# Kernel optimization log

Measured on AMD Instinct MI355X. Metric: run time of the kernel, lower is better.

## Reference

```python
import jax, jax.numpy as jnp
import numpy as np

B_SCENES = 2; K = 5; C = 128; H = 64; W = 64
D_INNER = C; D_STATE = 16; DT_RANK = 8
C_TUKEY = 0.3; ALPHA = 2.0; BETA = 0.4; GAMMA = 0.8


def affine_grid(theta, Ho, Wo):
    # torch F.affine_grid, align_corners=False (pixel centers)
    xs = (jnp.arange(Wo, dtype=jnp.float32) + 0.5) * (2.0 / Wo) - 1.0
    ys = (jnp.arange(Ho, dtype=jnp.float32) + 0.5) * (2.0 / Ho) - 1.0
    gx, gy = jnp.meshgrid(xs, ys)
    base = jnp.stack([gx, gy, jnp.ones_like(gx)], axis=-1)  # (H,W,3)
    return jnp.einsum('nij,hwj->nhwi', theta, base)  # (N,H,W,2)


def grid_sample(src, grid):
    # bilinear, zero padding, align_corners=False; src (N,C,H,W), grid (N,H,W,2)
    N, Cc, Hs, Ws = src.shape
    ix = ((grid[..., 0] + 1.0) * Ws - 1.0) * 0.5
    iy = ((grid[..., 1] + 1.0) * Hs - 1.0) * 0.5
    x0 = jnp.floor(ix); y0 = jnp.floor(iy)
    def tap(xf, yf):
        v = ((xf >= 0) & (xf <= Ws - 1) & (yf >= 0) & (yf <= Hs - 1)).astype(src.dtype)
        xc = jnp.clip(xf, 0, Ws - 1).astype(jnp.int32)
        yc = jnp.clip(yf, 0, Hs - 1).astype(jnp.int32)
        vals = jax.vmap(lambda s, y, x: s[:, y, x])(src, yc, xc)  # (N,C,H,W)
        return vals * v[:, None]
    wx1 = (ix - x0)[:, None]; wy1 = (iy - y0)[:, None]
    wx0 = 1.0 - wx1; wy0 = 1.0 - wy1
    return (tap(x0, y0) * wx0 * wy0 + tap(x0 + 1.0, y0) * wx1 * wy0
            + tap(x0, y0 + 1.0) * wx0 * wy1 + tap(x0 + 1.0, y0 + 1.0) * wx1 * wy1)


def ss2d(tokens, in_proj_w, conv_w, conv_b, x_proj_w, dt_w, dt_b, A_logs, Ds, ln_g, ln_b, out_proj_w):
    # tokens (C, Hs, Ws) channel-first; VMamba-style v05_noz core, d_inner=C
    xin = jnp.einsum('chw,dc->dhw', tokens, in_proj_w)
    xc = jax.lax.conv_general_dilated(xin[None], conv_w, (1, 1), [(1, 1), (1, 1)],
                                      dimension_numbers=('NCHW', 'OIHW', 'NCHW'),
                                      feature_group_count=D_INNER)[0] + conv_b[:, None, None]
    xa = jax.nn.silu(xc)
    d, Hs, Ws = xa.shape
    L = Hs * Ws
    x_hw = xa.reshape(d, L)
    x_wh = jnp.swapaxes(xa, 1, 2).reshape(d, L)
    xs = jnp.stack([x_hw, x_wh, x_hw[:, ::-1], x_wh[:, ::-1]], axis=0)  # (4,d,L)
    x_dbl = jnp.einsum('kdl,kcd->kcl', xs, x_proj_w)
    dt = x_dbl[:, :DT_RANK]
    Bm = x_dbl[:, DT_RANK:DT_RANK + D_STATE]
    Cm = x_dbl[:, DT_RANK + D_STATE:]
    dts = jax.nn.softplus(jnp.einsum('kdr,krl->kdl', dt_w, dt) + dt_b[..., None])
    A = -jnp.exp(A_logs)  # (4,d,n)
    seq = (jnp.moveaxis(xs, -1, 0), jnp.moveaxis(dts, -1, 0),
           jnp.moveaxis(Bm, -1, 0), jnp.moveaxis(Cm, -1, 0))
    def step(h, inp):
        xt, dtt, Bt, Ct = inp
        h = h * jnp.exp(dtt[..., None] * A) + (dtt * xt)[..., None] * Bt[:, None, :]
        return h, jnp.einsum('kdn,kn->kd', h, Ct)
    h0 = jnp.zeros((4, d, D_STATE), tokens.dtype)
    _, ys = jax.lax.scan(jax.checkpoint(step), h0, seq)  # ys (L,4,d)
    ys = jnp.moveaxis(ys, 0, -1) + Ds[..., None] * xs  # (4,d,L)
    untr = lambda y: jnp.swapaxes(y.reshape(d, Ws, Hs), 1, 2).reshape(d, L)
    y = ys[0] + untr(ys[1]) + ys[2][:, ::-1] + untr(ys[3][:, ::-1])
    yt = y.T  # (L,d)
    mu = yt.mean(-1, keepdims=True)
    var = ((yt - mu) ** 2).mean(-1, keepdims=True)
    yn = (yt - mu) * jax.lax.rsqrt(var + 1e-5) * ln_g + ln_b
    out = yn @ out_proj_w.T  # (L,C)
    return jnp.moveaxis(out.reshape(Hs, Ws, -1), -1, 0)  # (C,Hs,Ws)


def forward(x, nam, in_proj_w, conv_w, conv_b, x_proj_w, dt_w, dt_b, A_logs, Ds, ln_g, ln_b, out_proj_w):
    xg = x.reshape(B_SCENES, K, C, H, W)  # record_len is constant K
    t_rows = nam[:, 0]  # ego row i=0 of t_matrix: (B,K,2,3)
    def scene(xb, t_row):
        warped = grid_sample(xb, affine_grid(t_row, H, W))  # (K,C,H,W)
        ego = warped[0]
        # per-pixel cosine sim across channels (F.normalize(dim=0) on (C,HW) views)
        en = ego / jnp.maximum(jnp.sqrt((ego ** 2).sum(0, keepdims=True)), 1e-6)
        nb = warped / jnp.maximum(jnp.sqrt((warped ** 2).sum(1, keepdims=True)), 1e-6)
        sims = jnp.clip((en[None] * nb).sum(1), -1.0, 1.0)  # (K,H,W)
        r = jnp.maximum(1.0 - sims, 0.0)
        xr = jnp.maximum(r / C_TUKEY, 0.0)
        w_pix = jnp.maximum(jnp.maximum(1.0 - xr * xr, 0.0) ** 2, 1e-6)[:, None]  # (K,1,H,W)
        tx = t_row[:, 0, 2]; ty = t_row[:, 1, 2]
        yaw = jnp.abs(jnp.arctan2(t_row[:, 0, 1], t_row[:, 0, 0]))
        g = jax.nn.sigmoid(ALPHA - BETA * jnp.sqrt(tx ** 2 + ty ** 2) - GAMMA * yaw)  # (K,)
        logit = jnp.log(w_pix + 1e-8) + jnp.log(g + 1e-8)[:, None, None, None]
        alpha = jax.nn.softmax(logit, axis=0)  # softmax over K per pixel
        weighted = warped * alpha
        tokens = jnp.swapaxes(weighted.reshape(K, C, H * W), 0, 1)  # (C,K,HW)
        out = ss2d(tokens, in_proj_w, conv_w, conv_b, x_proj_w, dt_w, dt_b,
                   A_logs, Ds, ln_g, ln_b, out_proj_w)  # (C,K,HW)
        return jnp.swapaxes(out, 0, 1).reshape(K, C, W, H)[0]  # (C,W,H) as in original view
    return jax.vmap(scene)(xg, t_rows)


def setup_inputs() -> dict:
    key = jax.random.key(0)
    ks = jax.random.split(key, 10)
    x = jax.random.normal(ks[0], (B_SCENES * K, C, H, W), jnp.float32)
    record_len = jnp.full((B_SCENES,), K, dtype=jnp.int32)
    eye = jnp.broadcast_to(jnp.array([[1.0, 0.0, 0.0], [0.0, 1.0, 0.0]], jnp.float32),
                           (B_SCENES, K, K, 2, 3))
    nam = eye + 0.05 * jax.random.normal(ks[1], (B_SCENES, K, K, 2, 3), jnp.float32)
    in_proj_w = 0.05 * jax.random.normal(ks[2], (D_INNER, C), jnp.float32)
    conv_w = 0.1 * jax.random.normal(ks[3], (D_INNER, 1, 3, 3), jnp.float32)
    conv_b = jnp.zeros((D_INNER,), jnp.float32)
    x_proj_w = 0.05 * jax.random.normal(ks[4], (4, DT_RANK + 2 * D_STATE, D_INNER), jnp.float32)
    dt_w = 0.1 * jax.random.normal(ks[5], (4, D_INNER, DT_RANK), jnp.float32)
    dt_b = -4.6 + 0.5 * jax.random.normal(ks[6], (4, D_INNER), jnp.float32)
    A_logs = jnp.broadcast_to(jnp.log(jnp.arange(1, D_STATE + 1, dtype=jnp.float32)),
                              (4, D_INNER, D_STATE)) + jnp.zeros((4, D_INNER, D_STATE), jnp.float32)
    Ds = jnp.ones((4, D_INNER), jnp.float32)
    ln_g = jnp.ones((D_INNER,), jnp.float32)
    ln_b = jnp.zeros((D_INNER,), jnp.float32)
    out_proj_w = 0.05 * jax.random.normal(ks[7], (C, D_INNER), jnp.float32)
    return {"x": x, "record_len": record_len, "normalized_affine_matrix": nam,
            "in_proj_w": in_proj_w, "conv_w": conv_w, "conv_b": conv_b,
            "x_proj_w": x_proj_w, "dt_w": dt_w, "dt_b": dt_b, "A_logs": A_logs,
            "Ds": Ds, "ln_g": ln_g, "ln_b": ln_b, "out_proj_w": out_proj_w}


def reference(x, record_len, normalized_affine_matrix, in_proj_w, conv_w, conv_b,
              x_proj_w, dt_w, dt_b, A_logs, Ds, ln_g, ln_b, out_proj_w):
    # record_len is a constant (= K per scene) and only determines the static grouping
    return forward(x, normalized_affine_matrix, in_proj_w, conv_w, conv_b,
                   x_proj_w, dt_w, dt_b, A_logs, Ds, ln_g, ln_b, out_proj_w)
```

## Files before the change

kernel.cpp:

```cpp
#include <hip/hip_runtime.h>
#include <math.h>

#define B_S   2
#define PIX   4096
#define LL    20480
#define NS    16
#define RR    8
#define NCHK  512
#define LC    40
#define SUBS  10
#define NSUB  4
#define NGRP  32
#define GCH   16
#define K0CP  52

typedef float v2f __attribute__((ext_vector_type(2)));

__device__ __forceinline__ v2f pk_mul(v2f a, v2f b) {
  v2f d;
  asm("v_pk_mul_f32 %0, %1, %2" : "=v"(d) : "v"(a), "v"(b));
  return d;
}
#define PK_FMA_ACC(a, b, c) asm("v_pk_fma_f32 %0, %1, %2, %0" : "+v"(a) : "v"(b), "v"(c))
#define PK_DECAY(h, e, m) asm("v_pk_fma_f32 %0, %0, %1, %2" : "+v"(h) : "v"(e), "v"(m))

template<int K>
__device__ __forceinline__ int zmapT(int l) {
  if (K == 0) return l;
  if (K == 1) return ((l % 5) << 12) + l / 5;
  if (K == 2) return 20479 - l;
  int lr = 20479 - l;
  return ((lr % 5) << 12) + lr / 5;
}

__global__ __launch_bounds__(256)
void k_warp(const float* __restrict__ x, const float* __restrict__ nam,
            float* __restrict__ warped) {
  int g = blockIdx.x * 256 + threadIdx.x;
  int p  = g & 4095;
  int c  = (g >> 12) & 127;
  int bk = g >> 19;
  int b = bk / 5, k = bk - b * 5;
  const float* th = nam + (size_t)(b * 25 + k) * 6;
  float gx = ((p & 63) + 0.5f) * 0.03125f - 1.0f;
  float gy = ((p >> 6) + 0.5f) * 0.03125f - 1.0f;
  float grx = th[0] * gx + th[1] * gy + th[2];
  float gry = th[3] * gx + th[4] * gy + th[5];
  float ix = ((grx + 1.0f) * 64.0f - 1.0f) * 0.5f;
  float iy = ((gry + 1.0f) * 64.0f - 1.0f) * 0.5f;
  float x0 = floorf(ix), y0 = floorf(iy);
  float fx = ix - x0,  fy = iy - y0;
  const float* src = x + (size_t)(bk * 128 + c) * PIX;
  float acc = 0.0f;
  #pragma unroll
  for (int dy = 0; dy < 2; ++dy) {
    float yf = y0 + dy;
    float wy = dy ? fy : 1.0f - fy;
    if (yf < 0.0f || yf > 63.0f) continue;
    int yi = (int)yf;
    #pragma unroll
    for (int dx = 0; dx < 2; ++dx) {
      float xf = x0 + dx;
      float wx = dx ? fx : 1.0f - fx;
      if (xf < 0.0f || xf > 63.0f) continue;
      acc += wx * wy * src[yi * 64 + (int)xf];
    }
  }
  warped[g] = acc;
}

__global__ __launch_bounds__(512)
void k_alpha(const float* __restrict__ warped, const float* __restrict__ nam,
             float* __restrict__ alpha) {
  __shared__ float part[8][64][9];
  int blk = blockIdx.x;
  int b = blk >> 6;
  int p0 = (blk & 63) << 6;
  int wv = threadIdx.x >> 6, lane = threadIdx.x & 63;
  int p = p0 + lane;
  const float* wb = warped + (size_t)b * 5 * 128 * PIX + p;
  float dot[5] = {0,0,0,0,0}, ssq[5] = {0,0,0,0,0};
  int c0 = wv * 16;
  for (int c = c0; c < c0 + 16; ++c) {
    float w0 = wb[(size_t)c * PIX];
    ssq[0] += w0 * w0;
    #pragma unroll
    for (int k = 1; k < 5; ++k) {
      float wk = wb[((size_t)k * 128 + c) * PIX];
      dot[k] += w0 * wk;
      ssq[k] += wk * wk;
    }
  }
  part[wv][lane][0] = ssq[0];
  #pragma unroll
  for (int k = 1; k < 5; ++k) {
    part[wv][lane][k] = dot[k];
    part[wv][lane][4 + k] = ssq[k];
  }
  __syncthreads();
  if (threadIdx.x < 64) {
    float q[9];
    #pragma unroll
    for (int j = 0; j < 9; ++j) {
      float s = 0.0f;
      #pragma unroll
      for (int w = 0; w < 8; ++w) s += part[w][lane][j];
      q[j] = s;
    }
    float n0 = fmaxf(sqrtf(q[0]), 1e-6f);
    float logit[5];
    #pragma unroll
    for (int k = 0; k < 5; ++k) {
      float dotk = (k == 0) ? q[0] : q[k];
      float ssqk = (k == 0) ? q[0] : q[4 + k];
      float nk = fmaxf(sqrtf(ssqk), 1e-6f);
      float sim = fminf(fmaxf(dotk / (n0 * nk), -1.0f), 1.0f);
      float r = fmaxf(1.0f - sim, 0.0f);
      float xr = r * (1.0f / 0.3f);
      float tt = fmaxf(1.0f - xr * xr, 0.0f);
      float wp = fmaxf(tt * tt, 1e-6f);
      const float* th = nam + (size_t)(b * 25 + k) * 6;
      float tx = th[2], ty = th[5];
      float yaw = fabsf(atan2f(th[1], th[0]));
      float gk = 1.0f / (1.0f + __expf(-(2.0f - 0.4f * sqrtf(tx*tx + ty*ty) - 0.8f * yaw)));
      logit[k] = __logf(wp + 1e-8f) + __logf(gk + 1e-8f);
    }
    float m = logit[0];
    #pragma unroll
    for (int k = 1; k < 5; ++k) m = fmaxf(m, logit[k]);
    float e[5], s = 0.0f;
    #pragma unroll
    for (int k = 0; k < 5; ++k) { e[k] = __expf(logit[k] - m); s += e[k]; }
    float inv = 1.0f / s;
    #pragma unroll
    for (int k = 0; k < 5; ++k)
      alpha[((size_t)(b * 5 + k)) * PIX + p] = e[k] * inv;
  }
}

__global__ __launch_bounds__(256, 4)
void k_gemm_in(const float* __restrict__ warped, const float* __restrict__ alpha,
               const float* __restrict__ W, float* __restrict__ X0) {
  __shared__ float xl[64][129];
  __shared__ __align__(16) float wlT[32][132];
  int t = threadIdx.x;
  int row0 = blockIdx.x * 64;
  int b = row0 / LL;
  int z0 = row0 - b * LL;
  int a = z0 >> 12;
  int p0 = z0 & 4095;
  int ba = b * 5 + a;
  int r = t & 63, cg = t >> 6;
  float av = alpha[(size_t)ba * PIX + p0 + r];
  #pragma unroll
  for (int i = 0; i < 32; ++i) {
    int c = cg * 32 + i;
    xl[r][c] = warped[((size_t)ba * 128 + c) * PIX + p0 + r] * av;
  }
  int zl2 = t & 31;
  int mg  = t >> 5;
  float acc0[16], acc1[16];
  #pragma unroll
  for (int i = 0; i < 16; ++i) { acc0[i] = 0.0f; acc1[i] = 0.0f; }
  for (int c0 = 0; c0 < 128; c0 += 32) {
    __syncthreads();
    #pragma unroll
    for (int i = 0; i < 16; ++i) {
      int m = (t >> 5) * 16 + i;
      wlT[t & 31][m] = W[(size_t)m * 128 + c0 + (t & 31)];
    }
    __syncthreads();
    const float* xr0 = xl[2 * zl2];
    const float* xr1 = xl[2 * zl2 + 1];
    for (int cc = 0; cc < 32; ++cc) {
      float xv0 = xr0[c0 + cc];
      float xv1 = xr1[c0 + cc];
      const float4* wr = (const float4*)(&wlT[cc][mg * 16]);
      #pragma unroll
      for (int q = 0; q < 4; ++q) {
        float4 w4 = wr[q];
        acc0[q*4+0] = fmaf(w4.x, xv0, acc0[q*4+0]);
        acc0[q*4+1] = fmaf(w4.y, xv0, acc0[q*4+1]);
        acc0[q*4+2] = fmaf(w4.z, xv0, acc0[q*4+2]);
        acc0[q*4+3] = fmaf(w4.w, xv0, acc0[q*4+3]);
        acc1[q*4+0] = fmaf(w4.x, xv1, acc1[q*4+0]);
        acc1[q*4+1] = fmaf(w4.y, xv1, acc1[q*4+1]);
        acc1[q*4+2] = fmaf(w4.z, xv1, acc1[q*4+2]);
        acc1[q*4+3] = fmaf(w4.w, xv1, acc1[q*4+3]);
      }
    }
  }
  __syncthreads();
  #pragma unroll
  for (int q = 0; q < 16; ++q) {
    xl[2 * zl2][mg * 16 + q] = acc0[q];
    xl[2 * zl2 + 1][mg * 16 + q] = acc1[q];
  }
  __syncthreads();
  #pragma unroll
  for (int i = 0; i < 32; ++i) {
    int idx = i * 256 + t;
    X0[((size_t)row0 + (idx >> 7)) * 128 + (idx & 127)] = xl[idx >> 7][idx & 127];
  }
}

__global__ __launch_bounds__(256)
void k_conv(const float* __restrict__ X0, const float* __restrict__ cw,
            const float* __restrict__ cb, float* __restrict__ XT) {
  int g = blockIdx.x * 256 + threadIdx.x;
  int d = g & 127;
  int zz4 = g >> 7;
  int b = zz4 / (LL / 4);
  int r = zz4 - b * (LL / 4);
  int z0 = r * 4;
  int a = z0 >> 12, p = z0 & 4095;
  float w9[9];
  #pragma unroll
  for (int i = 0; i < 9; ++i) w9[i] = cw[d * 9 + i];
  float cbv = cb[d];
  float acc[4] = {cbv, cbv, cbv, cbv};
  #pragma unroll
  for (int di = 0; di < 3; ++di) {
    int aa = a + di - 1;
    if (aa < 0 || aa >= 5) continue;
    const float* rowb = X0 + ((size_t)b * LL + (size_t)aa * PIX) * 128 + d;
    #pragma unroll
    for (int dj = -1; dj <= 4; ++dj) {
      int pp = p + dj;
      if (pp < 0 || pp >= PIX) continue;
      float v = rowb[(size_t)pp * 128];
      #pragma unroll
      for (int o = 0; o < 4; ++o) {
        int rel = dj - o;
        if (rel >= -1 && rel <= 1) acc[o] = fmaf(w9[di * 3 + rel + 1], v, acc[o]);
      }
    }
  }
  float* dst = XT + (size_t)(zz4 * 4) * 128 + d;
  #pragma unroll
  for (int o = 0; o < 4; ++o) {
    float sg = 1.0f / (1.0f + __expf(-acc[o]));
    dst[(size_t)o * 128] = acc[o] * sg;
  }
}

__global__ __launch_bounds__(256, 4)
void k_gemmZ(const float* __restrict__ X, const float* __restrict__ W,
             float* __restrict__ ZdtB, float* __restrict__ ZC) {
  __shared__ float xl[64][129];
  __shared__ __align__(16) float wlT[32][164];
  int t = threadIdx.x;
  int row0 = blockIdx.x * 64;
  #pragma unroll
  for (int i = 0; i < 32; ++i) {
    int idx = i * 256 + t;
    xl[idx >> 7][idx & 127] = X[((size_t)row0 + (idx >> 7)) * 128 + (idx & 127)];
  }
  int zl2 = t & 31;
  int mg  = t >> 5;
  float acc0[20], acc1[20];
  #pragma unroll
  for (int i = 0; i < 20; ++i) { acc0[i] = 0.0f; acc1[i] = 0.0f; }
  for (int c0 = 0; c0 < 128; c0 += 32) {
    __syncthreads();
    #pragma unroll
    for (int i = 0; i < 20; ++i) {
      int m = (t >> 5) * 20 + i;
      wlT[t & 31][m] = W[(size_t)m * 128 + c0 + (t & 31)];
    }
    __syncthreads();
    const float* xr0 = xl[2 * zl2];
    const float* xr1 = xl[2 * zl2 + 1];
    for (int cc = 0; cc < 32; ++cc) {
      float xv0 = xr0[c0 + cc];
      float xv1 = xr1[c0 + cc];
      const float4* wr = (const float4*)(&wlT[cc][mg * 20]);
      #pragma unroll
      for (int q = 0; q < 5; ++q) {
        float4 w4 = wr[q];
        acc0[q*4+0] = fmaf(w4.x, xv0, acc0[q*4+0]);
        acc0[q*4+1] = fmaf(w4.y, xv0, acc0[q*4+1]);
        acc0[q*4+2] = fmaf(w4.z, xv0, acc0[q*4+2]);
        acc0[q*4+3] = fmaf(w4.w, xv0, acc0[q*4+3]);
        acc1[q*4+0] = fmaf(w4.x, xv1, acc1[q*4+0]);
        acc1[q*4+1] = fmaf(w4.y, xv1, acc1[q*4+1]);
        acc1[q*4+2] = fmaf(w4.z, xv1, acc1[q*4+2]);
        acc1[q*4+3] = fmaf(w4.w, xv1, acc1[q*4+3]);
      }
    }
  }
  int dir = mg >> 1;
  int halfc = mg & 1;
  #pragma unroll
  for (int rr = 0; rr < 2; ++rr) {
    const float* acc = rr ? acc1 : acc0;
    int row = row0 + 2 * zl2 + rr;
    int b = row / LL, z = row - b * LL;
    int a = z >> 12, qq = z & 4095;
    int l;
    if (dir == 0)      l = z;
    else if (dir == 1) l = 5 * qq + a;
    else if (dir == 2) l = 20479 - z;
    else               l = 20479 - (5 * qq + a);
    size_t seqrow = (size_t)(b * 4 + dir) * LL + l;
    if (halfc == 0) {
      float* dD = ZdtB + seqrow * 24;
      #pragma unroll
      for (int q2 = 0; q2 < 5; ++q2)
        *(float4*)(dD + q2 * 4) = make_float4(acc[q2*4], acc[q2*4+1], acc[q2*4+2], acc[q2*4+3]);
    } else {
      float* dD = ZdtB + seqrow * 24;
      *(float4*)(dD + 20) = make_float4(acc[0], acc[1], acc[2], acc[3]);
      float* dC = ZC + seqrow * 16;
      #pragma unroll
      for (int q2 = 0; q2 < 4; ++q2)
        *(float4*)(dC + q2 * 4) = make_float4(acc[4+q2*4], acc[4+q2*4+1], acc[4+q2*4+2], acc[4+q2*4+3]);
    }
  }
}

template<int K>
__device__ void scan_body(int b, int chunk, int dh, int lane,
    const float* __restrict__ XT, const float* __restrict__ ZdtB,
    const float* __restrict__ ZC,
    const float* __restrict__ dt_w, const float* __restrict__ dt_b,
    const float* __restrict__ A_logs, const float* __restrict__ Ds,
    float* __restrict__ h_out, float* __restrict__ sumdts,
    float* __restrict__ ysz, float* __restrict__ cumdtv,
    float* stD, float* stC, float* xs)
{
  const int d = dh * 64 + lane;
  const int kd = K * 128 + d;
  bool chainok = true;
  #pragma unroll
  for (int n = 0; n < NS; ++n) {
    float An = -__expf(A_logs[(size_t)kd * 16 + n]);
    chainok = chainok && (fabsf(An + (float)(n + 1)) < 3e-5f * (float)(n + 1));
  }
  v2f dw2[4];
  #pragma unroll
  for (int r = 0; r < 4; ++r) {
    dw2[r][0] = dt_w[(size_t)kd * 8 + 2 * r];
    dw2[r][1] = dt_w[(size_t)kd * 8 + 2 * r + 1];
  }
  const float dtb = dt_b[kd], dsv = Ds[kd];
  v2f h2[8];
  #pragma unroll
  for (int n = 0; n < 8; ++n) h2[n] = (v2f){0.0f, 0.0f};
  float sdt = 0.0f;
  const int seq = b * 4 + K;
  const float* ZDs = ZdtB + (size_t)seq * LL * 24;
  const float* ZCs = ZC + (size_t)seq * LL * 16;
  const float* Xb = XT + (size_t)b * LL * 128;
  float* ysb = ysz + (size_t)seq * PIX * 128;
  float* cdb = cumdtv + (size_t)seq * PIX * 128;
  const int l0 = chunk * LC;

  if (__all(chainok ? 1 : 0)) {
    #pragma unroll 1
    for (int sub = 0; sub < NSUB; ++sub) {
      const int ls = l0 + sub * SUBS;
      {
        const v2f* srcD = (const v2f*)(ZDs + (size_t)ls * 24);
        v2f* dstD = (v2f*)stD;
        #pragma unroll
        for (int i = 0; i < 2; ++i) {
          int idx = i * 64 + lane;
          if (idx < SUBS * 12) dstD[idx] = srcD[idx];
        }
      }
      int s0c = 0;
      bool needC;
      if (K == 0)      needC = (ls < PIX);
      else if (K == 2) needC = (ls + SUBS > LL - PIX);
      else             needC = true;
      if (K == 1) s0c = (5 - (ls % 5)) % 5;
      if (K == 3) s0c = (9 - (ls % 5)) % 5;
      if (needC) {
        if (K == 0 || K == 2) {
          const v2f* srcC = (const v2f*)(ZCs + (size_t)ls * 16);
          v2f* dstC = (v2f*)stC;
          #pragma unroll
          for (int i = 0; i < 2; ++i) {
            int idx = i * 64 + lane;
            if (idx < SUBS * 8) dstC[idx] = srcC[idx];
          }
        } else {
          int j = lane >> 4, col = lane & 15;
          if (j < 2) {
            int l = ls + s0c + 5 * j;
            if (l > LL - 1) l = LL - 1;
            stC[lane] = ZCs[(size_t)l * 16 + col];
          }
        }
      }
      #pragma unroll
      for (int s = 0; s < SUBS; ++s) {
        int z = zmapT<K>(ls + s);
        xs[s * 64 + lane] = Xb[(size_t)z * 128 + d];
      }
      int zc = 0;
      if (K == 1) zc = (ls + s0c) / 5;
      if (K == 3) zc = (20479 - ls - s0c) / 5;
      int yj = 0;
      #pragma unroll
      for (int s = 0; s < SUBS; ++s) {
        const v2f* rowD = (const v2f*)(stD + s * 24);
        v2f zd0 = rowD[0], zd1 = rowD[1], zd2 = rowD[2], zd3 = rowD[3];
        v2f da = pk_mul(dw2[0], zd0);
        PK_FMA_ACC(da, dw2[1], zd1);
        PK_FMA_ACC(da, dw2[2], zd2);
        PK_FMA_ACC(da, dw2[3], zd3);
        float dtl = dtb + da[0] + da[1];
        float edt = __expf(dtl);
        float e1 = __builtin_amdgcn_rcpf(1.0f + edt);
        float dt = (dtl > 20.0f) ? dtl : __logf(1.0f + edt);
        sdt += dt;
        float xsv = xs[s * 64 + lane];
        float dtx = dt * xsv;
        v2f dtx2 = {dtx, dtx};
        float e2 = e1 * e1;
        v2f E[8];
        E[0] = (v2f){e1, e2};
        v2f e2s = {e2, e2};
        E[1] = pk_mul(E[0], e2s);
        E[2] = pk_mul(E[1], e2s);
        E[3] = pk_mul(E[2], e2s);
        float e8 = E[3][1];
        v2f e8s = {e8, e8};
        E[4] = pk_mul(E[0], e8s);
        E[5] = pk_mul(E[1], e8s);
        E[6] = pk_mul(E[2], e8s);
        E[7] = pk_mul(E[3], e8s);
        const v2f* B2 = (const v2f*)(stD + s * 24 + 8);
        #pragma unroll
        for (int i = 0; i < 8; ++i) {
          v2f m = pk_mul(dtx2, B2[i]);
          PK_DECAY(h2[i], E[i], m);
        }
        bool doY;
        int z;
        if (K == 0)      { z = ls + s;            doY = (z < PIX); }
        else if (K == 2) { z = 20479 - (ls + s);  doY = (z < PIX); }
        else             { z = zc;                doY = ((s % 5) == s0c); }
        if (doY) {
          const v2f* C2 = (const v2f*)(stC + ((K == 0 || K == 2) ? s : yj) * 16);
          v2f ya = pk_mul(h2[0], C2[0]);
          #pragma unroll
          for (int i = 1; i < 8; ++i) PK_FMA_ACC(ya, h2[i], C2[i]);
          float y = fmaf(dsv, xsv, ya[0] + ya[1]);
          size_t o = (size_t)z * 128 + d;
          ysb[o] = y;
          cdb[o] = sdt;
          ++yj;
          if (K == 1) ++zc;
          if (K == 3) --zc;
        }
      }
    }
  } else {
    float An[NS];
    #pragma unroll
    for (int n = 0; n < NS; ++n) An[n] = -__expf(A_logs[(size_t)kd * 16 + n]);
    float hs[NS];
    #pragma unroll
    for (int n = 0; n < NS; ++n) hs[n] = 0.0f;
    #pragma unroll 1
    for (int l = l0; l < l0 + LC; ++l) {
      int z = zmapT<K>(l);
      const float* rowD = ZDs + (size_t)l * 24;
      float dtl = dtb;
      #pragma unroll
      for (int r = 0; r < RR; ++r) dtl += dt_w[(size_t)kd * 8 + r] * rowD[r];
      float edt = __expf(dtl);
      float dt = (dtl > 20.0f) ? dtl : __logf(1.0f + edt);
      sdt += dt;
      float xv = Xb[(size_t)z * 128 + d];
      float dtx = dt * xv;
      #pragma unroll
      for (int n = 0; n < NS; ++n)
        hs[n] = hs[n] * __expf(dt * An[n]) + dtx * rowD[8 + n];
      if (z < PIX) {
        const float* rowC = ZCs + (size_t)l * 16;
        float y = dsv * xv;
        #pragma unroll
        for (int n = 0; n < NS; ++n) y = fmaf(hs[n], rowC[n], y);
        size_t o = (size_t)z * 128 + d;
        ysb[o] = y;
        cdb[o] = sdt;
      }
    }
    #pragma unroll
    for (int n = 0; n < 8; ++n) h2[n] = (v2f){hs[2*n], hs[2*n+1]};
  }
  float* ho = h_out + (((size_t)seq * NCHK + chunk) * 128 + d) * 16;
  #pragma unroll
  for (int n = 0; n < 8; ++n) {
    ho[2*n] = h2[n][0];
    ho[2*n+1] = h2[n][1];
  }
  sumdts[((size_t)seq * NCHK + chunk) * 128 + d] = sdt;
}

__global__ __launch_bounds__(256, 6)
void k_scan1(const float* __restrict__ XT, const float* __restrict__ ZdtB,
             const float* __restrict__ ZC,
             const float* __restrict__ dt_w, const float* __restrict__ dt_b,
             const float* __restrict__ A_logs, const float* __restrict__ Ds,
             float* __restrict__ h_out, float* __restrict__ sumdts,
             float* __restrict__ ysz, float* __restrict__ cumdtv) {
  __shared__ __align__(16) float stD_all[4][SUBS * 24];
  __shared__ __align__(16) float stC_all[4][SUBS * 16];
  __shared__ __align__(16) float xs_all[4][SUBS * 64];
  int tid = threadIdx.x, wid = tid >> 6, lane = tid & 63;
  int bid = blockIdx.x;
  int bb = bid / (K0CP + 768);
  int idx = bid - bb * (K0CP + 768);
  int k, cp;
  if (idx < K0CP)            { k = 0; cp = idx; }
  else if (idx < K0CP + 256) { k = 1; cp = idx - K0CP; }
  else if (idx < K0CP + 512) { k = 2; cp = idx - (K0CP + 256); }
  else                       { k = 3; cp = idx - (K0CP + 512); }
  int chunk = cp * 2 + (wid >> 1);
  int dh = wid & 1;
  float* stD = stD_all[wid];
  float* stC = stC_all[wid];
  float* xs  = xs_all[wid];
  switch (k) {
    case 0: scan_body<0>(bb, chunk, dh, lane, XT, ZdtB, ZC, dt_w, dt_b, A_logs, Ds, h_out, sumdts, ysz, cumdtv, stD, stC, xs); break;
    case 1: scan_body<1>(bb, chunk, dh, lane, XT, ZdtB, ZC, dt_w, dt_b, A_logs, Ds, h_out, sumdts, ysz, cumdtv, stD, stC, xs); break;
    case 2: scan_body<2>(bb, chunk, dh, lane, XT, ZdtB, ZC, dt_w, dt_b, A_logs, Ds, h_out, sumdts, ysz, cumdtv, stD, stC, xs); break;
    default: scan_body<3>(bb, chunk, dh, lane, XT, ZdtB, ZC, dt_w, dt_b, A_logs, Ds, h_out, sumdts, ysz, cumdtv, stD, stC, xs); break;
  }
}

__global__ __launch_bounds__(256)
void k_comb_a(const float* __restrict__ A_logs, const float* __restrict__ sumdts,
              const float* __restrict__ h_out, float* __restrict__ Ag,
              float* __restrict__ Bg) {
  int g = blockIdx.x * 256 + threadIdx.x;
  int n = g & 15;
  int d = (g >> 4) & 127;
  int grp = (g >> 11) & 31;
  int seq = g >> 16;
  int k = seq & 3;
  float An = -__expf(A_logs[(size_t)(k * 128 + d) * 16 + n]);
  float A = 1.0f, Bv = 0.0f;
  size_t cbase = (size_t)seq * NCHK + grp * GCH;
  #pragma unroll 4
  for (int j = 0; j < GCH; ++j) {
    float a = __expf(An * sumdts[(cbase + j) * 128 + d]);
    float b = h_out[((cbase + j) * 128 + d) * 16 + n];
    A *= a;
    Bv = Bv * a + b;
  }
  size_t o = (((size_t)seq * NGRP + grp) * 128 + d) * 16 + n;
  Ag[o] = A;
  Bg[o] = Bv;
}

__global__ __launch_bounds__(256)
void k_comb_b(const float* __restrict__ Ag, const float* __restrict__ Bg,
              float* __restrict__ Hg) {
  int g = blockIdx.x * 256 + threadIdx.x;
  int n = g & 15;
  int d = (g >> 4) & 127;
  int seq = g >> 11;
  float H = 0.0f;
  #pragma unroll
  for (int grp = 0; grp < NGRP; ++grp) {
    size_t o = (((size_t)seq * NGRP + grp) * 128 + d) * 16 + n;
    Hg[o] = H;
    H = Ag[o] * H + Bg[o];
  }
}

__global__ __launch_bounds__(256)
void k_comb_c(const float* __restrict__ A_logs, const float* __restrict__ sumdts,
              const float* __restrict__ h_out, const float* __restrict__ Hg,
              float* __restrict__ h_in) {
  int g = blockIdx.x * 256 + threadIdx.x;
  int n = g & 15;
  int d = (g >> 4) & 127;
  int grp = (g >> 11) & 31;
  int seq = g >> 16;
  int k = seq & 3;
  float An = -__expf(A_logs[(size_t)(k * 128 + d) * 16 + n]);
  float h = Hg[(((size_t)seq * NGRP + grp) * 128 + d) * 16 + n];
  size_t cbase = (size_t)seq * NCHK + grp * GCH;
  #pragma unroll 4
  for (int j = 0; j < GCH; ++j) {
    size_t o = ((cbase + j) * 128 + d) * 16 + n;
    h_in[o] = h;
    float a = __expf(An * sumdts[(cbase + j) * 128 + d]);
    h = a * h + h_out[o];
  }
}

__global__ __launch_bounds__(256)
void k_wt(const float* __restrict__ Wo, float* __restrict__ WT) {
  __shared__ float tl[32][33];
  int bx = blockIdx.x & 3, by = blockIdx.x >> 2;
  int t = threadIdx.x;
  int tx = t & 31, ty = t >> 5;
  #pragma unroll
  for (int i = 0; i < 4; ++i)
    tl[ty + i * 8][tx] = Wo[(size_t)(by * 32 + ty + i * 8) * 128 + bx * 32 + tx];
  __syncthreads();
  #pragma unroll
  for (int i = 0; i < 4; ++i)
    WT[(size_t)(bx * 32 + ty + i * 8) * 128 + by * 32 + tx] = tl[tx][ty + i * 8];
}

__global__ __launch_bounds__(256)
void k_merge(const float* __restrict__ ysz, const float* __restrict__ ZC,
             const float* __restrict__ A_logs, const float* __restrict__ h_in,
             const float* __restrict__ cumdt,
             const float* __restrict__ ln_g, const float* __restrict__ ln_b,
             const float* __restrict__ WT, float* __restrict__ out) {
  __shared__ __align__(16) float ynT[128][20];
  __shared__ float red[4][8][2];
  int blk = blockIdx.x;
  int b = blk >> 8;
  int p0 = (blk & 255) * 16;
  int tid = threadIdx.x;
  int t = tid & 127;
  int half = tid >> 7;
  int w = tid >> 6;
  float g = ln_g[t], bb = ln_b[t];
  bool cok[4];
  #pragma unroll
  for (int k = 0; k < 4; ++k) {
    bool c = true;
    #pragma unroll
    for (int n = 0; n < NS; ++n) {
      float An = -__expf(A_logs[(size_t)(k * 128 + t) * 16 + n]);
      c = c && (fabsf(An + (float)(n + 1)) < 3e-5f * (float)(n + 1));
    }
    cok[k] = c;
  }
  float yv[8];
  #pragma unroll
  for (int i = 0; i < 8; ++i) {
    int p = p0 + 2 * i + half;
    float y = 0.0f;
    #pragma unroll
    for (int k = 0; k < 4; ++k) {
      size_t zi = ((size_t)(b * 4 + k) * PIX + p) * 128 + t;
      float yk = ysz[zi];
      int l;
      if (k == 0)      l = p;
      else if (k == 1) l = 5 * p;
      else if (k == 2) l = 20479 - p;
      else             l = 20479 - 5 * p;
      int chunk = l / LC;
      float cd = cumdt[zi];
      const v2f* hi2 = (const v2f*)(h_in + (((size_t)(b * 4 + k) * NCHK + chunk) * 128 + t) * 16);
      const v2f* Cr2 = (const v2f*)(ZC + ((size_t)(b * 4 + k) * LL + l) * 16);
      float fix;
      if (cok[k]) {
        float q = __expf(-cd);
        float q2 = q * q;
        v2f Q[8];
        Q[0] = (v2f){q, q2};
        v2f q2s = {q2, q2};
        Q[1] = pk_mul(Q[0], q2s);
        Q[2] = pk_mul(Q[1], q2s);
        Q[3] = pk_mul(Q[2], q2s);
        float q8 = Q[3][1];
        v2f q8s = {q8, q8};
        Q[4] = pk_mul(Q[0], q8s);
        Q[5] = pk_mul(Q[1], q8s);
        Q[6] = pk_mul(Q[2], q8s);
        Q[7] = pk_mul(Q[3], q8s);
        v2f a = pk_mul(pk_mul(hi2[0], Cr2[0]), Q[0]);
        #pragma unroll
        for (int j = 1; j < 8; ++j) {
          v2f m = pk_mul(hi2[j], Cr2[j]);
          PK_FMA_ACC(a, m, Q[j]);
        }
        fix = a[0] + a[1];
      } else {
        fix = 0.0f;
        const float* hi = (const float*)hi2;
        const float* Cr = (const float*)Cr2;
        #pragma unroll
        for (int n = 0; n < NS; ++n) {
          float An = -__expf(A_logs[(size_t)(k * 128 + t) * 16 + n]);
          fix += Cr[n] * hi[n] * __expf(An * cd);
        }
      }
      y += yk + fix;
    }
    yv[i] = y;
    float s1 = y, s2 = y * y;
    #pragma unroll
    for (int off = 32; off; off >>= 1) {
      s1 += __shfl_xor(s1, off);
      s2 += __shfl_xor(s2, off);
    }
    if ((tid & 63) == 0) { red[w][i][0] = s1; red[w][i][1] = s2; }
  }
  __syncthreads();
  #pragma unroll
  for (int i = 0; i < 8; ++i) {
    int pl = 2 * i + half;
    float S1 = red[half * 2][i][0] + red[half * 2 + 1][i][0];
    float S2 = red[half * 2][i][1] + red[half * 2 + 1][i][1];
    float mu = S1 * (1.0f / 128.0f);
    float var = S2 * (1.0f / 128.0f) - mu * mu;
    float rs = rsqrtf(var + 1e-5f);
    ynT[t][pl] = (yv[i] - mu) * rs * g + bb;
  }
  __syncthreads();
  float acc[8];
  #pragma unroll
  for (int i = 0; i < 8; ++i) acc[i] = 0.0f;
  for (int dd = 0; dd < 128; ++dd) {
    float wv = WT[(size_t)dd * 128 + t];
    const float4* yr = (const float4*)(&ynT[dd][half * 8]);
    float4 ya = yr[0], yb4 = yr[1];
    acc[0] = fmaf(ya.x,  wv, acc[0]);
    acc[1] = fmaf(ya.y,  wv, acc[1]);
    acc[2] = fmaf(ya.z,  wv, acc[2]);
    acc[3] = fmaf(ya.w,  wv, acc[3]);
    acc[4] = fmaf(yb4.x, wv, acc[4]);
    acc[5] = fmaf(yb4.y, wv, acc[5]);
    acc[6] = fmaf(yb4.z, wv, acc[6]);
    acc[7] = fmaf(yb4.w, wv, acc[7]);
  }
  float* dst = out + ((size_t)b * 128 + t) * PIX + p0 + half * 8;
  *(float4*)(dst)     = make_float4(acc[0], acc[1], acc[2], acc[3]);
  *(float4*)(dst + 4) = make_float4(acc[4], acc[5], acc[6], acc[7]);
}

extern "C" void kernel_launch(void* const* d_in, const int* in_sizes, int n_in,
                              void* d_out, int out_size, void* d_ws, size_t ws_size,
                              hipStream_t stream) {
  const float* x         = (const float*)d_in[0];
  const float* nam       = (const float*)d_in[2];
  const float* in_proj_w = (const float*)d_in[3];
  const float* conv_w    = (const float*)d_in[4];
  const float* conv_b    = (const float*)d_in[5];
  const float* x_proj_w  = (const float*)d_in[6];
  const float* dt_w      = (const float*)d_in[7];
  const float* dt_b      = (const float*)d_in[8];
  const float* A_logs    = (const float*)d_in[9];
  const float* Ds        = (const float*)d_in[10];
  const float* ln_g      = (const float*)d_in[11];
  const float* ln_b      = (const float*)d_in[12];
  const float* out_proj_w= (const float*)d_in[13];
  float* out = (float*)d_out;
  float* ws  = (float*)d_ws;

  float* warped = ws;
  float* alpha  = warped + 5242880;
  float* X0     = alpha  + 40960;
  float* XT     = X0     + 5242880;
  float* ZdtB   = XT     + 5242880;
  float* ZC     = ZdtB   + 3932160;
  float* sums   = ZC     + 2621440;
  float* ysz    = sums   + 524288;
  float* cumdt  = ysz    + 4194304;
  float* WT     = cumdt  + 4194304;
  float* Ag     = WT     + 16384;
  float* Bg     = Ag     + 524288;
  float* Hg     = Bg     + 524288;

  float* h_out = ws;
  float* h_in  = XT;

  k_warp   <<<20480, 256, 0, stream>>>(x, nam, warped);
  k_alpha  <<<128,   512, 0, stream>>>(warped, nam, alpha);
  k_gemm_in<<<640,   256, 0, stream>>>(warped, alpha, in_proj_w, X0);
  k_conv   <<<5120,  256, 0, stream>>>(X0, conv_w, conv_b, XT);
  k_gemmZ  <<<640,   256, 0, stream>>>(XT, x_proj_w, ZdtB, ZC);
  k_scan1  <<<B_S * (K0CP + 768), 256, 0, stream>>>(XT, ZdtB, ZC, dt_w, dt_b,
                                                    A_logs, Ds, h_out, sums, ysz, cumdt);
  k_comb_a <<<2048,  256, 0, stream>>>(A_logs, sums, h_out, Ag, Bg);
  k_comb_b <<<64,    256, 0, stream>>>(Ag, Bg, Hg);
  k_comb_c <<<2048,  256, 0, stream>>>(A_logs, sums, h_out, Hg, h_in);
  k_wt     <<<16,    256, 0, stream>>>(out_proj_w, WT);
  k_merge  <<<512,   256, 0, stream>>>(ysz, ZC, A_logs, h_in, cumdt,
                                       ln_g, ln_b, WT, out);
}
```

Before: 256.8 us.

## Software-pipeline scan sub-chunk loads in registers and store cumulative decay instead of cumdt

The chunked scan now prefetches the next sub-chunk's dt/B/C rows and x values into registers (double-buffered) while computing the current one, replacing the LDS staging of x. It also stores the running product of exp(-dt) instead of the cumulative dt, so the merge kernel skips an exp (the fallback path recomputes the log). Launch bounds drop occupancy from 6 to 5 waves to make room for the extra registers. The intent is to hide global load latency in the scan, at the cost of higher register pressure and some precision drift from the running product.

```diff
diff --git a/kernel.cpp b/kernel.cpp
--- a/kernel.cpp
+++ b/kernel.cpp
@@ -319,6 +319,59 @@
   }
 }
 
+struct PF {
+  v2f D0, D1;
+  v2f C0, C1;
+  float cS;
+  float xr[SUBS];
+};
+
+template<int K>
+__device__ __forceinline__ void pf_load(int ls, int lane, int d,
+    const float* __restrict__ ZDs, const float* __restrict__ ZCs,
+    const float* __restrict__ Xb, PF& pf) {
+  const v2f* srcD = (const v2f*)(ZDs + (size_t)ls * 24);
+  pf.D0 = srcD[lane];
+  if (lane < SUBS * 12 - 64) pf.D1 = srcD[64 + lane];
+  if (K == 0 || K == 2) {
+    bool needC = (K == 0) ? (ls < PIX) : (ls + SUBS > LL - PIX);
+    if (needC) {
+      const v2f* srcC = (const v2f*)(ZCs + (size_t)ls * 16);
+      pf.C0 = srcC[lane];
+      if (lane < SUBS * 8 - 64) pf.C1 = srcC[64 + lane];
+    }
+  } else {
+    if (lane < 32) {
+      int s0c = (K == 1) ? (5 - (ls % 5)) % 5 : (9 - (ls % 5)) % 5;
+      int j = lane >> 4, col = lane & 15;
+      int l = ls + s0c + 5 * j;
+      if (l > LL - 1) l = LL - 1;
+      pf.cS = ZCs[(size_t)l * 16 + col];
+    }
+  }
+  #pragma unroll
+  for (int s = 0; s < SUBS; ++s) {
+    int z = zmapT<K>(ls + s);
+    pf.xr[s] = Xb[(size_t)z * 128 + d];
+  }
+}
+
+template<int K>
+__device__ __forceinline__ void pf_store(int ls, int lane, const PF& pf,
+                                         float* stD, float* stC) {
+  ((v2f*)stD)[lane] = pf.D0;
+  if (lane < SUBS * 12 - 64) ((v2f*)stD)[64 + lane] = pf.D1;
+  if (K == 0 || K == 2) {
+    bool needC = (K == 0) ? (ls < PIX) : (ls + SUBS > LL - PIX);
+    if (needC) {
+      ((v2f*)stC)[lane] = pf.C0;
+      if (lane < SUBS * 8 - 64) ((v2f*)stC)[64 + lane] = pf.C1;
+    }
+  } else {
+    if (lane < 32) stC[lane] = pf.cS;
+  }
+}
+
 template<int K>
 __device__ void scan_body(int b, int chunk, int dh, int lane,
     const float* __restrict__ XT, const float* __restrict__ ZdtB,
@@ -326,8 +379,8 @@
     const float* __restrict__ dt_w, const float* __restrict__ dt_b,
     const float* __restrict__ A_logs, const float* __restrict__ Ds,
     float* __restrict__ h_out, float* __restrict__ sumdts,
-    float* __restrict__ ysz, float* __restrict__ cumdtv,
-    float* stD, float* stC, float* xs)
+    float* __restrict__ ysz, float* __restrict__ cumqv,
+    float* stD, float* stC)
 {
   const int d = dh * 64 + lane;
   const int kd = K * 128 + d;
@@ -348,57 +401,20 @@
   #pragma unroll
   for (int n = 0; n < 8; ++n) h2[n] = (v2f){0.0f, 0.0f};
   float sdt = 0.0f;
+  float qrun = 1.0f;
   const int seq = b * 4 + K;
   const float* ZDs = ZdtB + (size_t)seq * LL * 24;
   const float* ZCs = ZC + (size_t)seq * LL * 16;
   const float* Xb = XT + (size_t)b * LL * 128;
   float* ysb = ysz + (size_t)seq * PIX * 128;
-  float* cdb = cumdtv + (size_t)seq * PIX * 128;
+  float* cqb = cumqv + (size_t)seq * PIX * 128;
   const int l0 = chunk * LC;
 
   if (__all(chainok ? 1 : 0)) {
-    #pragma unroll 1
-    for (int sub = 0; sub < NSUB; ++sub) {
-      const int ls = l0 + sub * SUBS;
-      {
-        const v2f* srcD = (const v2f*)(ZDs + (size_t)ls * 24);
-        v2f* dstD = (v2f*)stD;
-        #pragma unroll
-        for (int i = 0; i < 2; ++i) {
-          int idx = i * 64 + lane;
-          if (idx < SUBS * 12) dstD[idx] = srcD[idx];
-        }
-      }
+    auto compute = [&](int ls, const float* xr) {
       int s0c = 0;
-      bool needC;
-      if (K == 0)      needC = (ls < PIX);
-      else if (K == 2) needC = (ls + SUBS > LL - PIX);
-      else             needC = true;
       if (K == 1) s0c = (5 - (ls % 5)) % 5;
       if (K == 3) s0c = (9 - (ls % 5)) % 5;
-      if (needC) {
-        if (K == 0 || K == 2) {
-          const v2f* srcC = (const v2f*)(ZCs + (size_t)ls * 16);
-          v2f* dstC = (v2f*)stC;
-          #pragma unroll
-          for (int i = 0; i < 2; ++i) {
-            int idx = i * 64 + lane;
-            if (idx < SUBS * 8) dstC[idx] = srcC[idx];
-          }
-        } else {
-          int j = lane >> 4, col = lane & 15;
-          if (j < 2) {
-            int l = ls + s0c + 5 * j;
-            if (l > LL - 1) l = LL - 1;
-            stC[lane] = ZCs[(size_t)l * 16 + col];
-          }
-        }
-      }
-      #pragma unroll
-      for (int s = 0; s < SUBS; ++s) {
-        int z = zmapT<K>(ls + s);
-        xs[s * 64 + lane] = Xb[(size_t)z * 128 + d];
-      }
       int zc = 0;
       if (K == 1) zc = (ls + s0c) / 5;
       if (K == 3) zc = (20479 - ls - s0c) / 5;
@@ -416,7 +432,8 @@
         float e1 = __builtin_amdgcn_rcpf(1.0f + edt);
         float dt = (dtl > 20.0f) ? dtl : __logf(1.0f + edt);
         sdt += dt;
-        float xsv = xs[s * 64 + lane];
+        qrun *= e1;
+        float xsv = xr[s];
         float dtx = dt * xsv;
         v2f dtx2 = {dtx, dtx};
         float e2 = e1 * e1;
@@ -451,12 +468,26 @@
           float y = fmaf(dsv, xsv, ya[0] + ya[1]);
           size_t o = (size_t)z * 128 + d;
           ysb[o] = y;
-          cdb[o] = sdt;
+          cqb[o] = qrun;
           ++yj;
           if (K == 1) ++zc;
           if (K == 3) --zc;
         }
       }
+    };
+    PF A, B;
+    pf_load<K>(l0, lane, d, ZDs, ZCs, Xb, A);
+    #pragma unroll
+    for (int pr = 0; pr < NSUB / 2; ++pr) {
+      int lsA = l0 + (2 * pr) * SUBS;
+      int lsB = lsA + SUBS;
+      pf_store<K>(lsA, lane, A, stD, stC);
+      pf_load<K>(lsB, lane, d, ZDs, ZCs, Xb, B);
+      compute(lsA, A.xr);
+      pf_store<K>(lsB, lane, B, stD, stC);
+      if (pr + 1 < NSUB / 2)
+        pf_load<K>(lsB + SUBS, lane, d, ZDs, ZCs, Xb, A);
+      compute(lsB, B.xr);
     }
   } else {
     float An[NS];
@@ -487,7 +518,7 @@
         for (int n = 0; n < NS; ++n) y = fmaf(hs[n], rowC[n], y);
         size_t o = (size_t)z * 128 + d;
         ysb[o] = y;
-        cdb[o] = sdt;
+        cqb[o] = __expf(-sdt);
       }
     }
     #pragma unroll
@@ -502,16 +533,15 @@
   sumdts[((size_t)seq * NCHK + chunk) * 128 + d] = sdt;
 }
 
-__global__ __launch_bounds__(256, 6)
+__global__ __launch_bounds__(256, 5)
 void k_scan1(const float* __restrict__ XT, const float* __restrict__ ZdtB,
              const float* __restrict__ ZC,
              const float* __restrict__ dt_w, const float* __restrict__ dt_b,
              const float* __restrict__ A_logs, const float* __restrict__ Ds,
              float* __restrict__ h_out, float* __restrict__ sumdts,
-             float* __restrict__ ysz, float* __restrict__ cumdtv) {
+             float* __restrict__ ysz, float* __restrict__ cumqv) {
   __shared__ __align__(16) float stD_all[4][SUBS * 24];
   __shared__ __align__(16) float stC_all[4][SUBS * 16];
-  __shared__ __align__(16) float xs_all[4][SUBS * 64];
   int tid = threadIdx.x, wid = tid >> 6, lane = tid & 63;
   int bid = blockIdx.x;
   int bb = bid / (K0CP + 768);
@@ -525,12 +555,11 @@
   int dh = wid & 1;
   float* stD = stD_all[wid];
   float* stC = stC_all[wid];
-  float* xs  = xs_all[wid];
   switch (k) {
-    case 0: scan_body<0>(bb, chunk, dh, lane, XT, ZdtB, ZC, dt_w, dt_b, A_logs, Ds, h_out, sumdts, ysz, cumdtv, stD, stC, xs); break;
-    case 1: scan_body<1>(bb, chunk, dh, lane, XT, ZdtB, ZC, dt_w, dt_b, A_logs, Ds, h_out, sumdts, ysz, cumdtv, stD, stC, xs); break;
-    case 2: scan_body<2>(bb, chunk, dh, lane, XT, ZdtB, ZC, dt_w, dt_b, A_logs, Ds, h_out, sumdts, ysz, cumdtv, stD, stC, xs); break;
-    default: scan_body<3>(bb, chunk, dh, lane, XT, ZdtB, ZC, dt_w, dt_b, A_logs, Ds, h_out, sumdts, ysz, cumdtv, stD, stC, xs); break;
+    case 0: scan_body<0>(bb, chunk, dh, lane, XT, ZdtB, ZC, dt_w, dt_b, A_logs, Ds, h_out, sumdts, ysz, cumqv, stD, stC); break;
+    case 1: scan_body<1>(bb, chunk, dh, lane, XT, ZdtB, ZC, dt_w, dt_b, A_logs, Ds, h_out, sumdts, ysz, cumqv, stD, stC); break;
+    case 2: scan_body<2>(bb, chunk, dh, lane, XT, ZdtB, ZC, dt_w, dt_b, A_logs, Ds, h_out, sumdts, ysz, cumqv, stD, stC); break;
+    default: scan_body<3>(bb, chunk, dh, lane, XT, ZdtB, ZC, dt_w, dt_b, A_logs, Ds, h_out, sumdts, ysz, cumqv, stD, stC); break;
   }
 }
 
@@ -615,7 +644,7 @@
 __global__ __launch_bounds__(256)
 void k_merge(const float* __restrict__ ysz, const float* __restrict__ ZC,
              const float* __restrict__ A_logs, const float* __restrict__ h_in,
-             const float* __restrict__ cumdt,
+             const float* __restrict__ cumq,
              const float* __restrict__ ln_g, const float* __restrict__ ln_b,
              const float* __restrict__ WT, float* __restrict__ out) {
   __shared__ __align__(16) float ynT[128][20];
@@ -654,12 +683,11 @@
       else if (k == 2) l = 20479 - p;
       else             l = 20479 - 5 * p;
       int chunk = l / LC;
-      float cd = cumdt[zi];
+      float q = cumq[zi];
       const v2f* hi2 = (const v2f*)(h_in + (((size_t)(b * 4 + k) * NCHK + chunk) * 128 + t) * 16);
       const v2f* Cr2 = (const v2f*)(ZC + ((size_t)(b * 4 + k) * LL + l) * 16);
       float fix;
       if (cok[k]) {
-        float q = __expf(-cd);
         float q2 = q * q;
         v2f Q[8];
         Q[0] = (v2f){q, q2};
@@ -681,6 +709,7 @@
         }
         fix = a[0] + a[1];
       } else {
+        float cd = -__logf(q);
         fix = 0.0f;
         const float* hi = (const float*)hi2;
         const float* Cr = (const float*)Cr2;
@@ -761,8 +790,8 @@
   float* ZC     = ZdtB   + 3932160;
   float* sums   = ZC     + 2621440;
   float* ysz    = sums   + 524288;
-  float* cumdt  = ysz    + 4194304;
-  float* WT     = cumdt  + 4194304;
+  float* cumq   = ysz    + 4194304;
+  float* WT     = cumq   + 4194304;
   float* Ag     = WT     + 16384;
   float* Bg     = Ag     + 524288;
   float* Hg     = Bg     + 524288;
@@ -776,11 +805,11 @@
   k_conv   <<<5120,  256, 0, stream>>>(X0, conv_w, conv_b, XT);
   k_gemmZ  <<<640,   256, 0, stream>>>(XT, x_proj_w, ZdtB, ZC);
   k_scan1  <<<B_S * (K0CP + 768), 256, 0, stream>>>(XT, ZdtB, ZC, dt_w, dt_b,
-                                                    A_logs, Ds, h_out, sums, ysz, cumdt);
+                                                    A_logs, Ds, h_out, sums, ysz, cumq);
   k_comb_a <<<2048,  256, 0, stream>>>(A_logs, sums, h_out, Ag, Bg);
   k_comb_b <<<64,    256, 0, stream>>>(Ag, Bg, Hg);
   k_comb_c <<<2048,  256, 0, stream>>>(A_logs, sums, h_out, Hg, h_in);
   k_wt     <<<16,    256, 0, stream>>>(out_proj_w, WT);
-  k_merge  <<<512,   256, 0, stream>>>(ysz, ZC, A_logs, h_in, cumdt,
+  k_merge  <<<512,   256, 0, stream>>>(ysz, ZC, A_logs, h_in, cumq,
                                        ln_g, ln_b, WT, out);
 }
```

After: 334.2 us. 1.3x slower.

## Store cumulative decay instead of cumulative dt and skip unused combine groups

Applied to the files above, without the earlier changes.

The scan now keeps a running product of exp(-dt) and stores that per output pixel, so the merge kernel no longer computes an exp per tap. The fallback path recovers cd with a log. The combine kernels return early for chunk groups whose carried-in states are never read by the merge (direction 0 only uses early chunks, direction 2 only late ones). The sub-chunk loop in the scan is also fully unrolled. The running product can differ slightly in precision from exp of the sum, and the unrolling raises register pressure.

```diff
diff --git a/kernel.cpp b/kernel.cpp
--- a/kernel.cpp
+++ b/kernel.cpp
@@ -326,7 +326,7 @@
     const float* __restrict__ dt_w, const float* __restrict__ dt_b,
     const float* __restrict__ A_logs, const float* __restrict__ Ds,
     float* __restrict__ h_out, float* __restrict__ sumdts,
-    float* __restrict__ ysz, float* __restrict__ cumdtv,
+    float* __restrict__ ysz, float* __restrict__ cumqv,
     float* stD, float* stC, float* xs)
 {
   const int d = dh * 64 + lane;
@@ -348,16 +348,17 @@
   #pragma unroll
   for (int n = 0; n < 8; ++n) h2[n] = (v2f){0.0f, 0.0f};
   float sdt = 0.0f;
+  float qrun = 1.0f;
   const int seq = b * 4 + K;
   const float* ZDs = ZdtB + (size_t)seq * LL * 24;
   const float* ZCs = ZC + (size_t)seq * LL * 16;
   const float* Xb = XT + (size_t)b * LL * 128;
   float* ysb = ysz + (size_t)seq * PIX * 128;
-  float* cdb = cumdtv + (size_t)seq * PIX * 128;
+  float* cqb = cumqv + (size_t)seq * PIX * 128;
   const int l0 = chunk * LC;
 
   if (__all(chainok ? 1 : 0)) {
-    #pragma unroll 1
+    #pragma unroll
     for (int sub = 0; sub < NSUB; ++sub) {
       const int ls = l0 + sub * SUBS;
       {
@@ -416,6 +417,7 @@
         float e1 = __builtin_amdgcn_rcpf(1.0f + edt);
         float dt = (dtl > 20.0f) ? dtl : __logf(1.0f + edt);
         sdt += dt;
+        qrun *= e1;
         float xsv = xs[s * 64 + lane];
         float dtx = dt * xsv;
         v2f dtx2 = {dtx, dtx};
@@ -451,7 +453,7 @@
           float y = fmaf(dsv, xsv, ya[0] + ya[1]);
           size_t o = (size_t)z * 128 + d;
           ysb[o] = y;
-          cdb[o] = sdt;
+          cqb[o] = qrun;
           ++yj;
           if (K == 1) ++zc;
           if (K == 3) --zc;
@@ -487,7 +489,7 @@
         for (int n = 0; n < NS; ++n) y = fmaf(hs[n], rowC[n], y);
         size_t o = (size_t)z * 128 + d;
         ysb[o] = y;
-        cdb[o] = sdt;
+        cqb[o] = __expf(-sdt);
       }
     }
     #pragma unroll
@@ -508,7 +510,7 @@
              const float* __restrict__ dt_w, const float* __restrict__ dt_b,
              const float* __restrict__ A_logs, const float* __restrict__ Ds,
              float* __restrict__ h_out, float* __restrict__ sumdts,
-             float* __restrict__ ysz, float* __restrict__ cumdtv) {
+             float* __restrict__ ysz, float* __restrict__ cumqv) {
   __shared__ __align__(16) float stD_all[4][SUBS * 24];
   __shared__ __align__(16) float stC_all[4][SUBS * 16];
   __shared__ __align__(16) float xs_all[4][SUBS * 64];
@@ -527,10 +529,10 @@
   float* stC = stC_all[wid];
   float* xs  = xs_all[wid];
   switch (k) {
-    case 0: scan_body<0>(bb, chunk, dh, lane, XT, ZdtB, ZC, dt_w, dt_b, A_logs, Ds, h_out, sumdts, ysz, cumdtv, stD, stC, xs); break;
-    case 1: scan_body<1>(bb, chunk, dh, lane, XT, ZdtB, ZC, dt_w, dt_b, A_logs, Ds, h_out, sumdts, ysz, cumdtv, stD, stC, xs); break;
-    case 2: scan_body<2>(bb, chunk, dh, lane, XT, ZdtB, ZC, dt_w, dt_b, A_logs, Ds, h_out, sumdts, ysz, cumdtv, stD, stC, xs); break;
-    default: scan_body<3>(bb, chunk, dh, lane, XT, ZdtB, ZC, dt_w, dt_b, A_logs, Ds, h_out, sumdts, ysz, cumdtv, stD, stC, xs); break;
+    case 0: scan_body<0>(bb, chunk, dh, lane, XT, ZdtB, ZC, dt_w, dt_b, A_logs, Ds, h_out, sumdts, ysz, cumqv, stD, stC, xs); break;
+    case 1: scan_body<1>(bb, chunk, dh, lane, XT, ZdtB, ZC, dt_w, dt_b, A_logs, Ds, h_out, sumdts, ysz, cumqv, stD, stC, xs); break;
+    case 2: scan_body<2>(bb, chunk, dh, lane, XT, ZdtB, ZC, dt_w, dt_b, A_logs, Ds, h_out, sumdts, ysz, cumqv, stD, stC, xs); break;
+    default: scan_body<3>(bb, chunk, dh, lane, XT, ZdtB, ZC, dt_w, dt_b, A_logs, Ds, h_out, sumdts, ysz, cumqv, stD, stC, xs); break;
   }
 }
 
@@ -544,6 +546,7 @@
   int grp = (g >> 11) & 31;
   int seq = g >> 16;
   int k = seq & 3;
+  if (k == 0 && grp > 6) return;
   float An = -__expf(A_logs[(size_t)(k * 128 + d) * 16 + n]);
   float A = 1.0f, Bv = 0.0f;
   size_t cbase = (size_t)seq * NCHK + grp * GCH;
@@ -585,6 +588,8 @@
   int grp = (g >> 11) & 31;
   int seq = g >> 16;
   int k = seq & 3;
+  if (k == 0 && grp > 6) return;
+  if (k == 2 && grp < 25) return;
   float An = -__expf(A_logs[(size_t)(k * 128 + d) * 16 + n]);
   float h = Hg[(((size_t)seq * NGRP + grp) * 128 + d) * 16 + n];
   size_t cbase = (size_t)seq * NCHK + grp * GCH;
@@ -615,7 +620,7 @@
 __global__ __launch_bounds__(256)
 void k_merge(const float* __restrict__ ysz, const float* __restrict__ ZC,
              const float* __restrict__ A_logs, const float* __restrict__ h_in,
-             const float* __restrict__ cumdt,
+             const float* __restrict__ cumq,
              const float* __restrict__ ln_g, const float* __restrict__ ln_b,
              const float* __restrict__ WT, float* __restrict__ out) {
   __shared__ __align__(16) float ynT[128][20];
@@ -654,12 +659,11 @@
       else if (k == 2) l = 20479 - p;
       else             l = 20479 - 5 * p;
       int chunk = l / LC;
-      float cd = cumdt[zi];
+      float q = cumq[zi];
       const v2f* hi2 = (const v2f*)(h_in + (((size_t)(b * 4 + k) * NCHK + chunk) * 128 + t) * 16);
       const v2f* Cr2 = (const v2f*)(ZC + ((size_t)(b * 4 + k) * LL + l) * 16);
       float fix;
       if (cok[k]) {
-        float q = __expf(-cd);
         float q2 = q * q;
         v2f Q[8];
         Q[0] = (v2f){q, q2};
@@ -681,6 +685,7 @@
         }
         fix = a[0] + a[1];
       } else {
+        float cd = -__logf(q);
         fix = 0.0f;
         const float* hi = (const float*)hi2;
         const float* Cr = (const float*)Cr2;
@@ -761,8 +766,8 @@
   float* ZC     = ZdtB   + 3932160;
   float* sums   = ZC     + 2621440;
   float* ysz    = sums   + 524288;
-  float* cumdt  = ysz    + 4194304;
-  float* WT     = cumdt  + 4194304;
+  float* cumq   = ysz    + 4194304;
+  float* WT     = cumq   + 4194304;
   float* Ag     = WT     + 16384;
   float* Bg     = Ag     + 524288;
   float* Hg     = Bg     + 524288;
@@ -776,11 +781,11 @@
   k_conv   <<<5120,  256, 0, stream>>>(X0, conv_w, conv_b, XT);
   k_gemmZ  <<<640,   256, 0, stream>>>(XT, x_proj_w, ZdtB, ZC);
   k_scan1  <<<B_S * (K0CP + 768), 256, 0, stream>>>(XT, ZdtB, ZC, dt_w, dt_b,
-                                                    A_logs, Ds, h_out, sums, ysz, cumdt);
+                                                    A_logs, Ds, h_out, sums, ysz, cumq);
   k_comb_a <<<2048,  256, 0, stream>>>(A_logs, sums, h_out, Ag, Bg);
   k_comb_b <<<64,    256, 0, stream>>>(Ag, Bg, Hg);
   k_comb_c <<<2048,  256, 0, stream>>>(A_logs, sums, h_out, Hg, h_in);
   k_wt     <<<16,    256, 0, stream>>>(out_proj_w, WT);
-  k_merge  <<<512,   256, 0, stream>>>(ysz, ZC, A_logs, h_in, cumdt,
+  k_merge  <<<512,   256, 0, stream>>>(ysz, ZC, A_logs, h_in, cumq,
                                        ln_g, ln_b, WT, out);
 }
```

Result: slower. 324.5 us (+26.4%).
